# Performance work log

Measured on AMD Instinct MI355X. Metric: run time of the kernel, lower is better.

Reference implementation:

```python
import jax, jax.numpy as jnp
import numpy as np
from functools import reduce

N_QUBITS = 4
N_LAYERS = 2
DIM = 16  # 2**N_QUBITS
BATCH = 4194304


def _cnot_matrix(c, t):
    # 16x16 CNOT on 4 qubits; wire 0 is the most-significant bit (PennyLane convention)
    M = np.zeros((DIM, DIM), np.float32)
    for b in range(DIM):
        bits = [(b >> (N_QUBITS - 1 - w)) & 1 for w in range(N_QUBITS)]
        if bits[c]:
            bits[t] ^= 1
        b2 = sum(bit << (N_QUBITS - 1 - w) for w, bit in enumerate(bits))
        M[b2, b] = 1.0
    return M

# ring of CNOTs applied in order (0,1),(1,2),(2,3),(3,0); later gates multiply on the left
CNOT_RING = reduce(np.matmul, [_cnot_matrix(3, 0), _cnot_matrix(2, 3),
                               _cnot_matrix(1, 2), _cnot_matrix(0, 1)])

# Z eigenvalue of qubit i in computational-basis state b: +1 if bit==0 else -1
ZSIGNS = np.array([[1.0 - 2.0 * ((b >> (N_QUBITS - 1 - i)) & 1)
                    for i in range(N_QUBITS)] for b in range(DIM)], np.float32)


def setup_inputs() -> dict:
    key = jax.random.key(0)
    kx, kw = jax.random.split(key)
    x = jax.random.normal(kx, (BATCH, DIM), dtype=jnp.float32)
    weights = jax.random.uniform(kw, (N_LAYERS, N_QUBITS), dtype=jnp.float32) * (2.0 * np.pi)
    return {"x": x, "weights": weights}


def reference(x, weights):
    # AmplitudeEmbedding(normalize=True): state = x / ||x||  -> [B,16] real state vector
    state = x / jnp.linalg.norm(x, axis=1, keepdims=True)

    cnot_ring = jnp.asarray(CNOT_RING)
    zsigns = jnp.asarray(ZSIGNS)

    half = weights * 0.5
    c = jnp.cos(half)  # [L,Q]
    s = jnp.sin(half)

    for layer in range(N_LAYERS):
        # RY(theta) = [[cos, -sin],[sin, cos]]; kron over wires (wire 0 leftmost)
        rys = [jnp.stack([jnp.stack([c[layer, i], -s[layer, i]]),
                          jnp.stack([s[layer, i], c[layer, i]])])
               for i in range(N_QUBITS)]
        U = reduce(jnp.kron, rys)            # [16,16]
        U = cnot_ring @ U                    # RY layer then CNOT ring
        state = state @ U.T                  # batched state evolution [B,16]

    probs = state * state                    # real amplitudes -> probabilities
    return probs @ zsigns                    # [B,4] PauliZ expvals
```

## Files before the change

kernel.cpp:

```cpp
#include <hip/hip_runtime.h>
#include <math.h>


#define BATCH   4194304
#define BLOCKS  4096
#define TPB     256

__global__ void prep_cs_kernel(const float* __restrict__ w, float* __restrict__ cs) {
    int i = threadIdx.x;
    if (i < 8) {
        float h = 0.5f * w[i];
        cs[i]     = cosf(h);
        cs[i + 8] = sinf(h);
    }
}

__global__ __launch_bounds__(TPB) void qlayer_kernel(
        const float4* __restrict__ x,
        const float*  __restrict__ cs,
        float4*       __restrict__ out) {
    float C[8], S[8];
#pragma unroll
    for (int i = 0; i < 8; ++i) { C[i] = cs[i]; S[i] = cs[i + 8]; }

    const int nthreads = BLOCKS * TPB;
    int g = blockIdx.x * TPB + threadIdx.x;

    for (int r = g; r < BATCH; r += nthreads) {
        const float4* xp = x + (size_t)r * 4;
        float4 v0 = xp[0], v1 = xp[1], v2 = xp[2], v3 = xp[3];
        float a[16] = { v0.x, v0.y, v0.z, v0.w,  v1.x, v1.y, v1.z, v1.w,
                        v2.x, v2.y, v2.z, v2.w,  v3.x, v3.y, v3.z, v3.w };

#pragma unroll
        for (int l = 0; l < 2; ++l) {
#pragma unroll
            for (int w = 0; w < 4; ++w) {
                const int m = 8 >> w;
                float c = C[l * 4 + w], s = S[l * 4 + w];
#pragma unroll
                for (int b = 0; b < 16; ++b) {
                    if (!(b & m)) {
                        float lo = a[b], hi = a[b | m];
                        a[b]     = c * lo - s * hi;
                        a[b | m] = s * lo + c * hi;
                    }
                }
            }
            {
                float t[16];
#pragma unroll
                for (int b = 0; b < 16; ++b) t[b] = a[b ^ (((b >> 3) & 1) ? 4 : 0)];
#pragma unroll
                for (int b = 0; b < 16; ++b) a[b] = t[b];
#pragma unroll
                for (int b = 0; b < 16; ++b) t[b] = a[b ^ (((b >> 2) & 1) ? 2 : 0)];
#pragma unroll
                for (int b = 0; b < 16; ++b) a[b] = t[b];
#pragma unroll
                for (int b = 0; b < 16; ++b) t[b] = a[b ^ (((b >> 1) & 1) ? 1 : 0)];
#pragma unroll
                for (int b = 0; b < 16; ++b) a[b] = t[b];
#pragma unroll
                for (int b = 0; b < 16; ++b) t[b] = a[b ^ (((b >> 0) & 1) ? 8 : 0)];
#pragma unroll
                for (int b = 0; b < 16; ++b) a[b] = t[b];
            }
        }

        float p[16];
#pragma unroll
        for (int b = 0; b < 16; ++b) p[b] = a[b] * a[b];

        float T = 0.f;
#pragma unroll
        for (int b = 0; b < 16; ++b) T += p[b];

        float S0 = 0.f, S1 = 0.f, S2 = 0.f, S3 = 0.f;
#pragma unroll
        for (int b = 0; b < 16; ++b) {
            if ((b >> 3) & 1) S0 += p[b];
            if ((b >> 2) & 1) S1 += p[b];
            if ((b >> 1) & 1) S2 += p[b];
            if ((b >> 0) & 1) S3 += p[b];
        }

        float invT = 1.0f / T;
        out[r] = make_float4(1.f - 2.f * S0 * invT,
                             1.f - 2.f * S1 * invT,
                             1.f - 2.f * S2 * invT,
                             1.f - 2.f * S3 * invT);
    }
}

extern "C" void kernel_launch(void* const* d_in, const int* in_sizes, int n_in,
                              void* d_out, int out_size, void* d_ws, size_t ws_size,
                              hipStream_t stream) {
    const float* x  = (const float*)d_in[0];
    const float* w  = (const float*)d_in[1];
    float*       cs = (float*)d_ws;
    float4*      o4 = (float4*)d_out;

    prep_cs_kernel<<<1, 64, 0, stream>>>(w, cs);
    qlayer_kernel<<<BLOCKS, TPB, 0, stream>>>((const float4*)x, cs, o4);
}
```

Measured before the change: 379.2 us.

## Split each 16-amplitude state across two lanes using cross-lane shuffles

Each batch row is now handled by a pair of adjacent lanes, each holding 8 amplitudes. The wire-0 rotation, part of the CNOT permutation and the final reductions exchange values with __shfl_xor. Adjacent lanes load neighbouring float4s, which is meant to make global loads more coalesced than the old one-row-per-thread pattern with its 64-byte stride, and register pressure per thread also drops. In exchange the kernel does extra shuffle work and writes float2 outputs, and the batch loop now makes twice as many passes.

```diff
diff --git a/kernel.cpp b/kernel.cpp
--- a/kernel.cpp
+++ b/kernel.cpp
@@ -5,6 +5,7 @@
 #define BATCH   4194304
 #define BLOCKS  4096
 #define TPB     256
+#define PAIRS_PER_PASS (BLOCKS * (TPB / 2))
 
 __global__ void prep_cs_kernel(const float* __restrict__ w, float* __restrict__ cs) {
     int i = threadIdx.x;
@@ -15,81 +16,91 @@
     }
 }
 
+#define BFLY(lo, hi, c, s) do {                     \
+        float _l = (lo), _h = (hi);                 \
+        (lo) = fmaf(-(s), _h, (c) * _l);            \
+        (hi) = fmaf( (s), _l, (c) * _h);            \
+    } while (0)
+
 __global__ __launch_bounds__(TPB) void qlayer_kernel(
-        const float4* __restrict__ x,
+        const float4* __restrict__ x4,
         const float*  __restrict__ cs,
-        float4*       __restrict__ out) {
+        float2*       __restrict__ out2) {
     float C[8], S[8];
 #pragma unroll
     for (int i = 0; i < 8; ++i) { C[i] = cs[i]; S[i] = cs[i + 8]; }
 
-    const int nthreads = BLOCKS * TPB;
-    int g = blockIdx.x * TPB + threadIdx.x;
+    const int gid = blockIdx.x * TPB + threadIdx.x;
+    const int p   = gid & 1;
+    const float sgn = p ? 1.0f : -1.0f;
 
-    for (int r = g; r < BATCH; r += nthreads) {
-        const float4* xp = x + (size_t)r * 4;
-        float4 v0 = xp[0], v1 = xp[1], v2 = xp[2], v3 = xp[3];
-        float a[16] = { v0.x, v0.y, v0.z, v0.w,  v1.x, v1.y, v1.z, v1.w,
-                        v2.x, v2.y, v2.z, v2.w,  v3.x, v3.y, v3.z, v3.w };
+    for (int r = (gid >> 1); r < BATCH; r += PAIRS_PER_PASS) {
+        const float4 lo4 = x4[(size_t)r * 4 + 2 * p];
+        const float4 hi4 = x4[(size_t)r * 4 + 2 * p + 1];
+        float a0 = lo4.x, a1 = lo4.y, a2 = lo4.z, a3 = lo4.w;
+        float a4 = hi4.x, a5 = hi4.y, a6 = hi4.z, a7 = hi4.w;
 
 #pragma unroll
         for (int l = 0; l < 2; ++l) {
-#pragma unroll
-            for (int w = 0; w < 4; ++w) {
-                const int m = 8 >> w;
-                float c = C[l * 4 + w], s = S[l * 4 + w];
-#pragma unroll
-                for (int b = 0; b < 16; ++b) {
-                    if (!(b & m)) {
-                        float lo = a[b], hi = a[b | m];
-                        a[b]     = c * lo - s * hi;
-                        a[b | m] = s * lo + c * hi;
-                    }
-                }
+            const float c0 = C[4*l+0], s0 = S[4*l+0];
+            const float c1 = C[4*l+1], s1 = S[4*l+1];
+            const float c2 = C[4*l+2], s2 = S[4*l+2];
+            const float c3 = C[4*l+3], s3 = S[4*l+3];
+
+            {
+                const float ss = sgn * s0;
+                float b0 = __shfl_xor(a0, 1), b1 = __shfl_xor(a1, 1);
+                float b2 = __shfl_xor(a2, 1), b3 = __shfl_xor(a3, 1);
+                float b4 = __shfl_xor(a4, 1), b5 = __shfl_xor(a5, 1);
+                float b6 = __shfl_xor(a6, 1), b7 = __shfl_xor(a7, 1);
+                a0 = fmaf(ss, b0, c0 * a0); a1 = fmaf(ss, b1, c0 * a1);
+                a2 = fmaf(ss, b2, c0 * a2); a3 = fmaf(ss, b3, c0 * a3);
+                a4 = fmaf(ss, b4, c0 * a4); a5 = fmaf(ss, b5, c0 * a5);
+                a6 = fmaf(ss, b6, c0 * a6); a7 = fmaf(ss, b7, c0 * a7);
             }
+            BFLY(a0, a4, c1, s1); BFLY(a1, a5, c1, s1);
+            BFLY(a2, a6, c1, s1); BFLY(a3, a7, c1, s1);
+            BFLY(a0, a2, c2, s2); BFLY(a1, a3, c2, s2);
+            BFLY(a4, a6, c2, s2); BFLY(a5, a7, c2, s2);
+            BFLY(a0, a1, c3, s3); BFLY(a2, a3, c3, s3);
+            BFLY(a4, a5, c3, s3); BFLY(a6, a7, c3, s3);
+
             {
-                float t[16];
-#pragma unroll
-                for (int b = 0; b < 16; ++b) t[b] = a[b ^ (((b >> 3) & 1) ? 4 : 0)];
-#pragma unroll
-                for (int b = 0; b < 16; ++b) a[b] = t[b];
-#pragma unroll
-                for (int b = 0; b < 16; ++b) t[b] = a[b ^ (((b >> 2) & 1) ? 2 : 0)];
-#pragma unroll
-                for (int b = 0; b < 16; ++b) a[b] = t[b];
-#pragma unroll
-                for (int b = 0; b < 16; ++b) t[b] = a[b ^ (((b >> 1) & 1) ? 1 : 0)];
-#pragma unroll
-                for (int b = 0; b < 16; ++b) a[b] = t[b];
-#pragma unroll
-                for (int b = 0; b < 16; ++b) t[b] = a[b ^ (((b >> 0) & 1) ? 8 : 0)];
-#pragma unroll
-                for (int b = 0; b < 16; ++b) a[b] = t[b];
+                float n0 = p ? a4 : a0, n4 = p ? a0 : a4;
+                float n1 = p ? a5 : a1, n5 = p ? a1 : a5;
+                float n2 = p ? a6 : a2, n6 = p ? a2 : a6;
+                float n3 = p ? a7 : a3, n7 = p ? a3 : a7;
+                a0 = n0; a1 = n1; a2 = n2; a3 = n3;
+                a4 = n4; a5 = n5; a6 = n6; a7 = n7;
             }
+            { float t = a4; a4 = a6; a6 = t; t = a5; a5 = a7; a7 = t; }
+            { float t = a2; a2 = a3; a3 = t; t = a6; a6 = a7; a7 = t; }
+            a1 = __shfl_xor(a1, 1); a3 = __shfl_xor(a3, 1);
+            a5 = __shfl_xor(a5, 1); a7 = __shfl_xor(a7, 1);
         }
 
-        float p[16];
-#pragma unroll
-        for (int b = 0; b < 16; ++b) p[b] = a[b] * a[b];
+        const float q0 = a0*a0, q1 = a1*a1, q2 = a2*a2, q3 = a3*a3;
+        const float q4 = a4*a4, q5 = a5*a5, q6 = a6*a6, q7 = a7*a7;
 
-        float T = 0.f;
-#pragma unroll
-        for (int b = 0; b < 16; ++b) T += p[b];
+        const float Tloc = ((q0+q1)+(q2+q3)) + ((q4+q5)+(q6+q7));
+        const float PT   = __shfl_xor(Tloc, 1);
+        const float T    = Tloc + PT;
 
-        float S0 = 0.f, S1 = 0.f, S2 = 0.f, S3 = 0.f;
-#pragma unroll
-        for (int b = 0; b < 16; ++b) {
-            if ((b >> 3) & 1) S0 += p[b];
-            if ((b >> 2) & 1) S1 += p[b];
-            if ((b >> 1) & 1) S2 += p[b];
-            if ((b >> 0) & 1) S3 += p[b];
-        }
+        const float S0 = p ? Tloc : PT;
+        float s1l = (q4+q5)+(q6+q7);
+        float s2l = (q2+q3)+(q6+q7);
+        float s3l = (q1+q3)+(q5+q7);
+        const float S1 = s1l + __shfl_xor(s1l, 1);
+        const float S2 = s2l + __shfl_xor(s2l, 1);
+        const float S3 = s3l + __shfl_xor(s3l, 1);
 
-        float invT = 1.0f / T;
-        out[r] = make_float4(1.f - 2.f * S0 * invT,
-                             1.f - 2.f * S1 * invT,
-                             1.f - 2.f * S2 * invT,
-                             1.f - 2.f * S3 * invT);
+        const float invT = 1.0f / T;
+        const float o0 = 1.0f - 2.0f * S0 * invT;
+        const float o1 = 1.0f - 2.0f * S1 * invT;
+        const float o2 = 1.0f - 2.0f * S2 * invT;
+        const float o3 = 1.0f - 2.0f * S3 * invT;
+
+        out2[(size_t)2 * r + p] = p ? make_float2(o2, o3) : make_float2(o0, o1);
     }
 }
 
@@ -99,8 +110,8 @@
     const float* x  = (const float*)d_in[0];
     const float* w  = (const float*)d_in[1];
     float*       cs = (float*)d_ws;
-    float4*      o4 = (float4*)d_out;
+    float2*      o2 = (float2*)d_out;
 
     prep_cs_kernel<<<1, 64, 0, stream>>>(w, cs);
-    qlayer_kernel<<<BLOCKS, TPB, 0, stream>>>((const float4*)x, cs, o4);
+    qlayer_kernel<<<BLOCKS, TPB, 0, stream>>>((const float4*)x, cs, o2);
 }
```

Result: no change. 377.5 us (-0.5%).
